# Optimization experiments

Measured on AMD Instinct MI355X. Metric: run time of the kernel, lower is better.

## Reference

```python
import jax, jax.numpy as jnp
import numpy as np

B, T, C, H = 2, 2048, 1024, 16
HD = C // H  # 64


def setup_inputs() -> dict:
    key = jax.random.key(0)
    ks = jax.random.split(key, 5)
    x = jax.random.normal(ks[0], (B, T, C), jnp.float32)
    scale = 0.02
    Wq = jax.random.normal(ks[1], (C, C), jnp.float32) * scale
    Wk = jax.random.normal(ks[2], (C, C), jnp.float32) * scale
    Wv = jax.random.normal(ks[3], (C, C), jnp.float32) * scale
    Wo = jax.random.normal(ks[4], (C, C), jnp.float32) * scale
    # RoPE tables: freqs_cis = exp(i * pos * theta_j), theta_j = 10000^(-2j/HD)
    pos = jnp.arange(T, dtype=jnp.float32)
    theta = 10000.0 ** (-jnp.arange(0, HD, 2, dtype=jnp.float32) / HD)  # [HD/2]
    ang = pos[:, None] * theta[None, :]  # [T, HD/2]
    cos = jnp.cos(ang)
    sin = jnp.sin(ang)
    return {"x": x, "Wq": Wq, "Wk": Wk, "Wv": Wv, "Wo": Wo, "cos": cos, "sin": sin}


def _rope(t, cos, sin):
    # t: [B,T,H,HD]; pairs (even, odd) along last dim form complex numbers
    b, s, h, hd = t.shape
    tr = t.reshape(b, s, h, hd // 2, 2)
    t0, t1 = tr[..., 0], tr[..., 1]
    c = cos[None, :, None, :]  # [1,T,1,HD/2]
    sn = sin[None, :, None, :]
    o0 = t0 * c - t1 * sn
    o1 = t0 * sn + t1 * c
    return jnp.stack([o0, o1], axis=-1).reshape(b, s, h, hd)


def reference(x, Wq, Wk, Wv, Wo, cos, sin):
    b, t, c = x.shape
    h, hd = H, c // H
    q = (x @ Wq.T).reshape(b, t, h, hd)
    k = (x @ Wk.T).reshape(b, t, h, hd)
    v = (x @ Wv.T).reshape(b, t, h, hd)
    q = _rope(q, cos, sin)
    k = _rope(k, cos, sin)
    # explicit causal attention with full TxT score matrix (as in source)
    att = jnp.einsum("bthd,bshd->bhts", q, k) / jnp.sqrt(jnp.float32(hd))
    causal = jnp.tril(jnp.ones((t, t), dtype=bool))
    att = jnp.where(causal[None, None, :, :], att, -jnp.inf)
    att = jax.nn.softmax(att, axis=-1)
    out = jnp.einsum("bhts,bshd->bthd", att, v).reshape(b, t, c)
    return out @ Wo.T
```

## Files before the change

### kernel.cpp

```cpp
#include <hip/hip_runtime.h>
#include <cstdint>
#include <cstddef>


typedef __bf16 bf16;
typedef float  f32x4  __attribute__((ext_vector_type(4)));
typedef __bf16 bf16x4 __attribute__((ext_vector_type(4)));
typedef __bf16 bf16x8 __attribute__((ext_vector_type(8)));

constexpr int Bb = 2, Tt = 2048, Cc = 1024, Hh = 16;
constexpr int Mrows = Bb * Tt;
constexpr int NT = Tt / 64;
constexpr int BM = 128, BN = 128, BK = 64;
constexpr int LDS_ = 72;

#define GLOAD_LDS16(gp, lp)                                                      \
    __builtin_amdgcn_global_load_lds(                                            \
        (const __attribute__((address_space(1))) void*)(gp),                     \
        (__attribute__((address_space(3))) void*)(lp), 16, 0, 0)

#define QUAD_T(v0, v1, v2, v3, c2)                                               \
    {                                                                            \
        float e0 = (c2 & 1) ? v0 : v1, e1 = (c2 & 1) ? v2 : v3;                  \
        e0 = __shfl_xor(e0, 1); e1 = __shfl_xor(e1, 1);                          \
        if (c2 & 1) { v0 = e0; v2 = e1; } else { v1 = e0; v3 = e1; }             \
        float f0 = (c2 & 2) ? v0 : v2, f1 = (c2 & 2) ? v1 : v3;                  \
        f0 = __shfl_xor(f0, 2); f1 = __shfl_xor(f1, 2);                          \
        if (c2 & 2) { v0 = f0; v1 = f1; } else { v2 = f0; v3 = f1; }             \
    }

__global__ __launch_bounds__(256) void convert_k(const float* __restrict__ x,
                                                 const float* __restrict__ Wq,
                                                 const float* __restrict__ Wk,
                                                 const float* __restrict__ Wv,
                                                 const float* __restrict__ Wo,
                                                 const float* __restrict__ cosb,
                                                 const float* __restrict__ sinb,
                                                 bf16* __restrict__ xb,
                                                 bf16* __restrict__ Wqkv,
                                                 bf16* __restrict__ Wob,
                                                 float2* __restrict__ cs)
{
    constexpr size_t M1 = 1024 * 1024;
    if (blockIdx.x >= 4096) {
        int pi = ((blockIdx.x - 4096) * 256 + threadIdx.x) * 8;
#pragma unroll
        for (int u = 0; u < 8; ++u)
            cs[pi + u] = float2{cosb[pi + u], sinb[pi + u]};
        return;
    }
    size_t e = ((size_t)blockIdx.x * 256 + threadIdx.x) * 8;
    const float* src; bf16* dst; float sc = 1.0f;
    if (e < 4 * M1)      { src = x  + e;          dst = xb   + e; }
    else if (e < 5 * M1) { src = Wq + (e - 4*M1); dst = Wqkv + (e - 4*M1);
                           sc = 0.125f * 1.44269504088896f; }
    else if (e < 6 * M1) { src = Wk + (e - 5*M1); dst = Wqkv + M1 + (e - 5*M1); }
    else if (e < 7 * M1) { src = Wv + (e - 6*M1); dst = Wqkv + 2*M1 + (e - 6*M1); }
    else                 { src = Wo + (e - 7*M1); dst = Wob  + (e - 7*M1); }
    float4 v0 = *(const float4*)(src);
    float4 v1 = *(const float4*)(src + 4);
    bf16x8 t;
    t[0] = (bf16)(v0.x*sc); t[1] = (bf16)(v0.y*sc); t[2] = (bf16)(v0.z*sc); t[3] = (bf16)(v0.w*sc);
    t[4] = (bf16)(v1.x*sc); t[5] = (bf16)(v1.y*sc); t[6] = (bf16)(v1.z*sc); t[7] = (bf16)(v1.w*sc);
    *(bf16x8*)dst = t;
}

__global__ __launch_bounds__(256) void gemm_qkv(const bf16* __restrict__ A,
                                                const bf16* __restrict__ W,
                                                bf16* __restrict__ QK,
                                                bf16* __restrict__ Vt,
                                                const float2* __restrict__ cs)
{
    __shared__ bf16 As[BM * BK];
    __shared__ bf16 Ws[BN * BK];
    const int tid  = threadIdx.x;
    const int lane = tid & 63, wave = tid >> 6;
    const int wr = (wave >> 1) * 64, wc = (wave & 1) * 64;
    const int l16 = lane & 15, lq = lane >> 4;
    const int row0 = blockIdx.x * BM, col0 = blockIdx.y * BN;
    const int srow = lane >> 3, scol = (lane & 7) * 8;

    f32x4 acc[4][4];
#pragma unroll
    for (int i = 0; i < 4; ++i)
#pragma unroll
        for (int j = 0; j < 4; ++j) acc[i][j] = f32x4{0.f, 0.f, 0.f, 0.f};

    const bf16* Abase = A + (size_t)(row0 + wave * 8 + srow) * Cc + scol;
    const bf16* Wbase = W + (size_t)(col0 + wave * 8 + srow) * Cc + scol;

    for (int k0 = 0; k0 < Cc; k0 += BK) {
#pragma unroll
        for (int rnd = 0; rnd < 4; ++rnd) {
            const int rr = rnd * 32 + wave * 8;
            GLOAD_LDS16(Abase + (size_t)rnd * 32 * Cc + k0, &As[rr * BK]);
            GLOAD_LDS16(Wbase + (size_t)rnd * 32 * Cc + k0, &Ws[rr * BK]);
        }
        __syncthreads();
#pragma unroll
        for (int ks = 0; ks < BK / 32; ++ks) {
            bf16x8 af[4], bfr[4];
#pragma unroll
            for (int i = 0; i < 4; ++i)
                af[i] = *(const bf16x8*)(&As[(wr + i * 16 + l16) * BK + ks * 32 + lq * 8]);
#pragma unroll
            for (int j = 0; j < 4; ++j)
                bfr[j] = *(const bf16x8*)(&Ws[(wc + j * 16 + l16) * BK + ks * 32 + lq * 8]);
#pragma unroll
            for (int i = 0; i < 4; ++i)
#pragma unroll
                for (int j = 0; j < 4; ++j)
                    acc[i][j] = __builtin_amdgcn_mfma_f32_16x16x32_bf16(
                        af[i], bfr[j], acc[i][j], 0, 0, 0);
        }
        __syncthreads();
    }

    const int c2 = l16 & 3, g4 = (l16 >> 2) * 4;
    if (blockIdx.y < 16) {
#pragma unroll
        for (int i = 0; i < 4; ++i)
#pragma unroll
            for (int j = 0; j < 4; ++j) {
                float v0 = acc[i][j][0], v1 = acc[i][j][1];
                float v2 = acc[i][j][2], v3 = acc[i][j][3];
                QUAD_T(v0, v1, v2, v3, c2);
                const int row = row0 + wr + i * 16 + lq * 4 + c2;
                const int t   = row & (Tt - 1);
                const int colb = wc + j * 16 + g4;
                const int p0   = (colb & 63) >> 1;
                float4 cp = *(const float4*)(&cs[t * 32 + p0]);
                bf16x4 pk;
                pk[0] = (bf16)(v0 * cp.x - v1 * cp.y);
                pk[1] = (bf16)(v0 * cp.y + v1 * cp.x);
                pk[2] = (bf16)(v2 * cp.z - v3 * cp.w);
                pk[3] = (bf16)(v2 * cp.w + v3 * cp.z);
                *(bf16x4*)(&QK[(size_t)row * 2048 + col0 + colb]) = pk;
            }
    } else {
#pragma unroll
        for (int i = 0; i < 4; ++i)
#pragma unroll
            for (int j = 0; j < 4; ++j) {
                const int dfull = col0 - 2048 + wc + j * 16 + l16;
                const int h = dfull >> 6, d = dfull & 63;
                const int row = row0 + wr + i * 16 + lq * 4;
                const int b = row >> 11, t = row & (Tt - 1);
                bf16x4 pk;
                pk[0] = (bf16)acc[i][j][0]; pk[1] = (bf16)acc[i][j][1];
                pk[2] = (bf16)acc[i][j][2]; pk[3] = (bf16)acc[i][j][3];
                *(bf16x4*)(&Vt[((size_t)(b * 16 + h) * 64 + d) * (size_t)Tt + t]) = pk;
            }
    }
}

__global__ __launch_bounds__(256) void gemm_o(const bf16* __restrict__ A,
                                              const bf16* __restrict__ W,
                                              float* __restrict__ Out)
{
    __shared__ bf16 As[BM * BK];
    __shared__ bf16 Ws[64 * BK];
    const int tid  = threadIdx.x;
    const int lane = tid & 63, wave = tid >> 6;
    const int wr = (wave >> 1) * 64, wc = (wave & 1) * 32;
    const int l16 = lane & 15, lq = lane >> 4;
    const int row0 = blockIdx.x * BM, col0 = blockIdx.y * 64;
    const int srow = lane >> 3, scol = (lane & 7) * 8;

    f32x4 acc[4][2];
#pragma unroll
    for (int i = 0; i < 4; ++i)
#pragma unroll
        for (int j = 0; j < 2; ++j) acc[i][j] = f32x4{0.f, 0.f, 0.f, 0.f};

    const bf16* Abase = A + (size_t)(row0 + wave * 8 + srow) * Cc + scol;
    const bf16* Wbase = W + (size_t)(col0 + wave * 8 + srow) * Cc + scol;

    for (int k0 = 0; k0 < Cc; k0 += BK) {
#pragma unroll
        for (int rnd = 0; rnd < 4; ++rnd)
            GLOAD_LDS16(Abase + (size_t)rnd * 32 * Cc + k0, &As[(rnd * 32 + wave * 8) * BK]);
#pragma unroll
        for (int rnd = 0; rnd < 2; ++rnd)
            GLOAD_LDS16(Wbase + (size_t)rnd * 32 * Cc + k0, &Ws[(rnd * 32 + wave * 8) * BK]);
        __syncthreads();
#pragma unroll
        for (int ks = 0; ks < BK / 32; ++ks) {
            bf16x8 af[4], bfr[2];
#pragma unroll
            for (int i = 0; i < 4; ++i)
                af[i] = *(const bf16x8*)(&As[(wr + i * 16 + l16) * BK + ks * 32 + lq * 8]);
#pragma unroll
            for (int j = 0; j < 2; ++j)
                bfr[j] = *(const bf16x8*)(&Ws[(wc + j * 16 + l16) * BK + ks * 32 + lq * 8]);
#pragma unroll
            for (int i = 0; i < 4; ++i)
#pragma unroll
                for (int j = 0; j < 2; ++j)
                    acc[i][j] = __builtin_amdgcn_mfma_f32_16x16x32_bf16(
                        af[i], bfr[j], acc[i][j], 0, 0, 0);
        }
        __syncthreads();
    }
    const int c2 = l16 & 3, g4 = (l16 >> 2) * 4;
#pragma unroll
    for (int i = 0; i < 4; ++i)
#pragma unroll
        for (int j = 0; j < 2; ++j) {
            float v0 = acc[i][j][0], v1 = acc[i][j][1];
            float v2 = acc[i][j][2], v3 = acc[i][j][3];
            QUAD_T(v0, v1, v2, v3, c2);
            const int row = row0 + wr + i * 16 + lq * 4 + c2;
            const int col = col0 + wc + j * 16 + g4;
            *(float4*)(&Out[(size_t)row * Cc + col]) = float4{v0, v1, v2, v3};
        }
}

__global__ __launch_bounds__(256, 4) void attn_k(const bf16* __restrict__ QK,
                                                 const bf16* __restrict__ Vt,
                                                 bf16* __restrict__ O)
{
    __shared__ bf16 Ks[64 * LDS_];
    __shared__ bf16 Vs[64 * LDS_];
    const int tid = threadIdx.x;
    const int wv = tid >> 6, lane = tid & 63;
    const int l16 = lane & 15, lq = lane >> 4;
    const int bh = blockIdx.y, b = bh >> 4, h = bh & 15;
    const int kr = tid >> 2, c0 = (tid & 3) * 16;
    const int pr = 32 * (kr >> 5) + 16 * ((kr >> 2) & 1) + 4 * ((kr >> 3) & 3) + (kr & 3);

    const bf16* kcol = QK + 1024 + (size_t)(b * Tt + kr) * 2048 + h * 64 + c0;
    const bf16* vcol = Vt + ((size_t)bh * 64 + kr) * Tt + c0;

    for (int phase = 0; phase < 2; ++phase) {
        const int qt = phase ? blockIdx.x : (NT - 1 - blockIdx.x);

        const int qglob = qt * 64 + wv * 16 + l16;
        const bf16* qp = QK + (size_t)(b * Tt + qglob) * 2048 + h * 64;
        bf16x8 qf0 = *(const bf16x8*)(qp + lq * 8);
        bf16x8 qf1 = *(const bf16x8*)(qp + 32 + lq * 8);

        uint4 pk0 = *(const uint4*)(kcol);
        uint4 pk1 = *(const uint4*)(kcol + 8);
        uint4 pv0 = *(const uint4*)(vcol);
        uint4 pv1 = *(const uint4*)(vcol + 8);

        float l = 0.f;
        f32x4 o[4];
#pragma unroll
        for (int dt = 0; dt < 4; ++dt) o[dt] = f32x4{0.f, 0.f, 0.f, 0.f};

        for (int t = 0; t <= qt; ++t) {
            *(uint4*)(&Ks[pr * LDS_ + c0])     = pk0;
            *(uint4*)(&Ks[pr * LDS_ + c0 + 8]) = pk1;
            *(uint4*)(&Vs[kr * LDS_ + c0])     = pv0;
            *(uint4*)(&Vs[kr * LDS_ + c0 + 8]) = pv1;
            __syncthreads();
            if (t < qt) {
                const bf16* kn = kcol + (size_t)(t + 1) * 64 * 2048;
                const bf16* vn = vcol + (t + 1) * 64;
                pk0 = *(const uint4*)(kn);
                pk1 = *(const uint4*)(kn + 8);
                pv0 = *(const uint4*)(vn);
                pv1 = *(const uint4*)(vn + 8);
            }

            f32x4 s[4];
#pragma unroll
            for (int mt = 0; mt < 4; ++mt) s[mt] = f32x4{0.f, 0.f, 0.f, 0.f};
#pragma unroll
            for (int mt = 0; mt < 4; ++mt) {
                bf16x8 a0 = *(const bf16x8*)(&Ks[(mt * 16 + l16) * LDS_ + lq * 8]);
                s[mt] = __builtin_amdgcn_mfma_f32_16x16x32_bf16(a0, qf0, s[mt], 0, 0, 0);
            }
#pragma unroll
            for (int mt = 0; mt < 4; ++mt) {
                bf16x8 a1 = *(const bf16x8*)(&Ks[(mt * 16 + l16) * LDS_ + 32 + lq * 8]);
                s[mt] = __builtin_amdgcn_mfma_f32_16x16x32_bf16(a1, qf1, s[mt], 0, 0, 0);
            }
            if (t == qt) {
                const int qloc = wv * 16 + l16;
#pragma unroll
                for (int mt = 0; mt < 4; ++mt)
#pragma unroll
                    for (int r = 0; r < 4; ++r) {
                        int keyl = (mt >> 1) * 32 + lq * 8 + (mt & 1) * 4 + r;
                        if (keyl > qloc) s[mt][r] = -1e30f;
                    }
            }
            bf16x8 pb0, pb1;
#pragma unroll
            for (int mt = 0; mt < 4; ++mt)
#pragma unroll
                for (int r = 0; r < 4; ++r) {
                    float p = exp2f(s[mt][r]);
                    l += p;
                    s[mt][r] = p;
                }
#pragma unroll
            for (int r = 0; r < 4; ++r) {
                pb0[r]     = (bf16)s[0][r];
                pb0[4 + r] = (bf16)s[1][r];
                pb1[r]     = (bf16)s[2][r];
                pb1[4 + r] = (bf16)s[3][r];
            }
#pragma unroll
            for (int dt = 0; dt < 4; ++dt) {
                bf16x8 v0 = *(const bf16x8*)(&Vs[(dt * 16 + l16) * LDS_ + lq * 8]);
                o[dt] = __builtin_amdgcn_mfma_f32_16x16x32_bf16(v0, pb0, o[dt], 0, 0, 0);
            }
#pragma unroll
            for (int dt = 0; dt < 4; ++dt) {
                bf16x8 v1 = *(const bf16x8*)(&Vs[(dt * 16 + l16) * LDS_ + 32 + lq * 8]);
                o[dt] = __builtin_amdgcn_mfma_f32_16x16x32_bf16(v1, pb1, o[dt], 0, 0, 0);
            }
            __syncthreads();
        }
        l += __shfl_xor(l, 16);
        l += __shfl_xor(l, 32);
        float inv = 1.f / l;
        bf16* op = O + (size_t)(b * Tt + qglob) * Cc + h * 64;
#pragma unroll
        for (int dt = 0; dt < 4; ++dt) {
            bf16x4 pk;
#pragma unroll
            for (int r = 0; r < 4; ++r) pk[r] = (bf16)(o[dt][r] * inv);
            *(bf16x4*)(op + dt * 16 + lq * 4) = pk;
        }
    }
}

extern "C" void kernel_launch(void* const* d_in, const int* in_sizes, int n_in,
                              void* d_out, int out_size, void* d_ws, size_t ws_size,
                              hipStream_t stream)
{
    const float* x    = (const float*)d_in[0];
    const float* Wq   = (const float*)d_in[1];
    const float* Wk   = (const float*)d_in[2];
    const float* Wv   = (const float*)d_in[3];
    const float* Wo   = (const float*)d_in[4];
    const float* cosb = (const float*)d_in[5];
    const float* sinb = (const float*)d_in[6];

    constexpr size_t M1 = 1024 * 1024;
    bf16* base = (bf16*)d_ws;
    bf16*   xb   = base;
    bf16*   QK   = base + 4 * M1;
    bf16*   VtG  = base + 12 * M1;
    bf16*   Wqkv = base + 16 * M1;
    bf16*   Wob  = base + 19 * M1;
    float2* csT  = (float2*)(base + 20 * M1);
    bf16*   Ow   = xb;

    convert_k<<<4096 + 32, 256, 0, stream>>>(x, Wq, Wk, Wv, Wo, cosb, sinb,
                                             xb, Wqkv, Wob, csT);

    gemm_qkv<<<dim3(Mrows / BM, 3072 / BN), 256, 0, stream>>>(
        xb, Wqkv, QK, VtG, csT);

    attn_k<<<dim3(NT / 2, Bb * Hh), 256, 0, stream>>>(QK, VtG, Ow);

    gemm_o<<<dim3(Mrows / BM, Cc / 64), 256, 0, stream>>>(Ow, Wob, (float*)d_out);
}
```

Before: 203.2 us.

## Pre-tile GEMM operands into MFMA fragment order for contiguous LDS loads

The convert kernel now writes x, Wqkv and Wo in a blocked layout where each 128x64 (or 64x64) K-tile is contiguous and arranged in MFMA fragment order. The attention kernel writes its output in the same tiled layout. Both GEMMs can then fill LDS with fully contiguous 512-element segments, and fragment reads walk consecutive 16-byte slots. This is meant to remove strided global rows and LDS bank conflicts from the unpadded row-major tiles, at the cost of scattered reads in the convert step and a more complex attention store pattern.

New measurement: 174.6 us. 1.16x faster.

```diff
diff --git a/kernel.cpp b/kernel.cpp
--- a/kernel.cpp
+++ b/kernel.cpp
@@ -11,7 +11,6 @@
 constexpr int Bb = 2, Tt = 2048, Cc = 1024, Hh = 16;
 constexpr int Mrows = Bb * Tt;
 constexpr int NT = Tt / 64;
-constexpr int BM = 128, BN = 128, BK = 64;
 constexpr int LDS_ = 72;
 
 #define GLOAD_LDS16(gp, lp)                                                      \
@@ -41,7 +40,6 @@
                                                  bf16* __restrict__ Wob,
                                                  float2* __restrict__ cs)
 {
-    constexpr size_t M1 = 1024 * 1024;
     if (blockIdx.x >= 4096) {
         int pi = ((blockIdx.x - 4096) * 256 + threadIdx.x) * 8;
 #pragma unroll
@@ -49,14 +47,35 @@
             cs[pi + u] = float2{cosb[pi + u], sinb[pi + u]};
         return;
     }
-    size_t e = ((size_t)blockIdx.x * 256 + threadIdx.x) * 8;
+    uint32_t id = blockIdx.x * 256 + threadIdx.x;
     const float* src; bf16* dst; float sc = 1.0f;
-    if (e < 4 * M1)      { src = x  + e;          dst = xb   + e; }
-    else if (e < 5 * M1) { src = Wq + (e - 4*M1); dst = Wqkv + (e - 4*M1);
-                           sc = 0.125f * 1.44269504088896f; }
-    else if (e < 6 * M1) { src = Wk + (e - 5*M1); dst = Wqkv + M1 + (e - 5*M1); }
-    else if (e < 7 * M1) { src = Wv + (e - 6*M1); dst = Wqkv + 2*M1 + (e - 6*M1); }
-    else                 { src = Wo + (e - 7*M1); dst = Wob  + (e - 7*M1); }
+    if (id < 524288u) {
+        uint32_t tile = id >> 10, slot = id & 1023;
+        uint32_t row = (tile >> 4) * 128 + (slot >> 9) * 64 +
+                       ((slot >> 6) & 3) * 16 + (slot & 15);
+        uint32_t k = (tile & 15) * 64 + ((slot >> 8) & 1) * 32 + ((slot >> 4) & 3) * 8;
+        src = x + (size_t)row * 1024 + k;
+        dst = xb + (size_t)id * 8;
+    } else if (id < 917504u) {
+        uint32_t t2 = id - 524288u;
+        uint32_t tile = t2 >> 10, slot = t2 & 1023;
+        uint32_t n = (tile >> 4) * 128 + (slot >> 9) * 64 +
+                     ((slot >> 6) & 3) * 16 + (slot & 15);
+        uint32_t k = (tile & 15) * 64 + ((slot >> 8) & 1) * 32 + ((slot >> 4) & 3) * 8;
+        if (n < 1024)      { src = Wq + (size_t)n * 1024 + k;
+                             sc = 0.125f * 1.44269504088896f; }
+        else if (n < 2048)   src = Wk + (size_t)(n - 1024) * 1024 + k;
+        else                 src = Wv + (size_t)(n - 2048) * 1024 + k;
+        dst = Wqkv + (size_t)t2 * 8;
+    } else {
+        uint32_t t3 = id - 917504u;
+        uint32_t tile = t3 >> 9, slot = t3 & 511;
+        uint32_t n = (tile >> 4) * 64 + (slot >> 8) * 32 +
+                     ((slot >> 6) & 1) * 16 + (slot & 15);
+        uint32_t k = (tile & 15) * 64 + ((slot >> 7) & 1) * 32 + ((slot >> 4) & 3) * 8;
+        src = Wo + (size_t)n * 1024 + k;
+        dst = Wob + (size_t)t3 * 8;
+    }
     float4 v0 = *(const float4*)(src);
     float4 v1 = *(const float4*)(src + 4);
     bf16x8 t;
@@ -71,14 +90,14 @@
                                                 bf16* __restrict__ Vt,
                                                 const float2* __restrict__ cs)
 {
-    __shared__ bf16 As[BM * BK];
-    __shared__ bf16 Ws[BN * BK];
+    __shared__ bf16 As[8192];
+    __shared__ bf16 Ws[8192];
     const int tid  = threadIdx.x;
     const int lane = tid & 63, wave = tid >> 6;
-    const int wr = (wave >> 1) * 64, wc = (wave & 1) * 64;
+    const int rhw = wave >> 1, chw = wave & 1;
+    const int wr = rhw * 64, wc = chw * 64;
     const int l16 = lane & 15, lq = lane >> 4;
-    const int row0 = blockIdx.x * BM, col0 = blockIdx.y * BN;
-    const int srow = lane >> 3, scol = (lane & 7) * 8;
+    const int row0 = blockIdx.x * 128, col0 = blockIdx.y * 128;
 
     f32x4 acc[4][4];
 #pragma unroll
@@ -86,26 +105,28 @@
 #pragma unroll
         for (int j = 0; j < 4; ++j) acc[i][j] = f32x4{0.f, 0.f, 0.f, 0.f};
 
-    const bf16* Abase = A + (size_t)(row0 + wave * 8 + srow) * Cc + scol;
-    const bf16* Wbase = W + (size_t)(col0 + wave * 8 + srow) * Cc + scol;
-
-    for (int k0 = 0; k0 < Cc; k0 += BK) {
+    const bf16* At = A + (size_t)blockIdx.x * 16 * 8192;
+    const bf16* Wt = W + (size_t)blockIdx.y * 16 * 8192;
+
+    for (int kb = 0; kb < 16; ++kb) {
+        const bf16* at = At + kb * 8192;
+        const bf16* wt = Wt + kb * 8192;
 #pragma unroll
         for (int rnd = 0; rnd < 4; ++rnd) {
-            const int rr = rnd * 32 + wave * 8;
-            GLOAD_LDS16(Abase + (size_t)rnd * 32 * Cc + k0, &As[rr * BK]);
-            GLOAD_LDS16(Wbase + (size_t)rnd * 32 * Cc + k0, &Ws[rr * BK]);
+            const int seg = rnd * 4 + wave;
+            GLOAD_LDS16(at + seg * 512 + lane * 8, &As[seg * 512]);
+            GLOAD_LDS16(wt + seg * 512 + lane * 8, &Ws[seg * 512]);
         }
         __syncthreads();
 #pragma unroll
-        for (int ks = 0; ks < BK / 32; ++ks) {
+        for (int ks = 0; ks < 2; ++ks) {
             bf16x8 af[4], bfr[4];
 #pragma unroll
             for (int i = 0; i < 4; ++i)
-                af[i] = *(const bf16x8*)(&As[(wr + i * 16 + l16) * BK + ks * 32 + lq * 8]);
+                af[i] = *(const bf16x8*)(&As[(rhw * 512 + ks * 256 + i * 64 + lq * 16 + l16) * 8]);
 #pragma unroll
             for (int j = 0; j < 4; ++j)
-                bfr[j] = *(const bf16x8*)(&Ws[(wc + j * 16 + l16) * BK + ks * 32 + lq * 8]);
+                bfr[j] = *(const bf16x8*)(&Ws[(chw * 512 + ks * 256 + j * 64 + lq * 16 + l16) * 8]);
 #pragma unroll
             for (int i = 0; i < 4; ++i)
 #pragma unroll
@@ -158,14 +179,14 @@
                                               const bf16* __restrict__ W,
                                               float* __restrict__ Out)
 {
-    __shared__ bf16 As[BM * BK];
-    __shared__ bf16 Ws[64 * BK];
+    __shared__ bf16 As[8192];
+    __shared__ bf16 Ws[4096];
     const int tid  = threadIdx.x;
     const int lane = tid & 63, wave = tid >> 6;
-    const int wr = (wave >> 1) * 64, wc = (wave & 1) * 32;
+    const int rhw = wave >> 1, chw = wave & 1;
+    const int wr = rhw * 64, wc = chw * 32;
     const int l16 = lane & 15, lq = lane >> 4;
-    const int row0 = blockIdx.x * BM, col0 = blockIdx.y * 64;
-    const int srow = lane >> 3, scol = (lane & 7) * 8;
+    const int row0 = blockIdx.x * 128, col0 = blockIdx.y * 64;
 
     f32x4 acc[4][2];
 #pragma unroll
@@ -173,26 +194,32 @@
 #pragma unroll
         for (int j = 0; j < 2; ++j) acc[i][j] = f32x4{0.f, 0.f, 0.f, 0.f};
 
-    const bf16* Abase = A + (size_t)(row0 + wave * 8 + srow) * Cc + scol;
-    const bf16* Wbase = W + (size_t)(col0 + wave * 8 + srow) * Cc + scol;
-
-    for (int k0 = 0; k0 < Cc; k0 += BK) {
-#pragma unroll
-        for (int rnd = 0; rnd < 4; ++rnd)
-            GLOAD_LDS16(Abase + (size_t)rnd * 32 * Cc + k0, &As[(rnd * 32 + wave * 8) * BK]);
-#pragma unroll
-        for (int rnd = 0; rnd < 2; ++rnd)
-            GLOAD_LDS16(Wbase + (size_t)rnd * 32 * Cc + k0, &Ws[(rnd * 32 + wave * 8) * BK]);
+    const bf16* At = A + (size_t)blockIdx.x * 16 * 8192;
+    const bf16* Wt = W + (size_t)blockIdx.y * 16 * 4096;
+
+    for (int kb = 0; kb < 16; ++kb) {
+        const bf16* at = At + kb * 8192;
+        const bf16* wt = Wt + kb * 4096;
+#pragma unroll
+        for (int rnd = 0; rnd < 4; ++rnd) {
+            const int seg = rnd * 4 + wave;
+            GLOAD_LDS16(at + seg * 512 + lane * 8, &As[seg * 512]);
+        }
+#pragma unroll
+        for (int rnd = 0; rnd < 2; ++rnd) {
+            const int seg = rnd * 4 + wave;
+            GLOAD_LDS16(wt + seg * 512 + lane * 8, &Ws[seg * 512]);
+        }
         __syncthreads();
 #pragma unroll
-        for (int ks = 0; ks < BK / 32; ++ks) {
+        for (int ks = 0; ks < 2; ++ks) {
             bf16x8 af[4], bfr[2];
 #pragma unroll
             for (int i = 0; i < 4; ++i)
-                af[i] = *(const bf16x8*)(&As[(wr + i * 16 + l16) * BK + ks * 32 + lq * 8]);
+                af[i] = *(const bf16x8*)(&As[(rhw * 512 + ks * 256 + i * 64 + lq * 16 + l16) * 8]);
 #pragma unroll
             for (int j = 0; j < 2; ++j)
-                bfr[j] = *(const bf16x8*)(&Ws[(wc + j * 16 + l16) * BK + ks * 32 + lq * 8]);
+                bfr[j] = *(const bf16x8*)(&Ws[(chw * 256 + ks * 128 + j * 64 + lq * 16 + l16) * 8]);
 #pragma unroll
             for (int i = 0; i < 4; ++i)
 #pragma unroll
@@ -319,13 +346,16 @@
         l += __shfl_xor(l, 16);
         l += __shfl_xor(l, 32);
         float inv = 1.f / l;
-        bf16* op = O + (size_t)(b * Tt + qglob) * Cc + h * 64;
+        bf16* obase = O + ((size_t)(b * 16 + (qt >> 1)) * 16 + h) * 8192;
+        const int rh = qt & 1;
 #pragma unroll
         for (int dt = 0; dt < 4; ++dt) {
             bf16x4 pk;
 #pragma unroll
             for (int r = 0; r < 4; ++r) pk[r] = (bf16)(o[dt][r] * inv);
-            *(bf16x4*)(op + dt * 16 + lq * 4) = pk;
+            const int slot = rh * 512 + (dt >> 1) * 256 + wv * 64 +
+                             ((dt & 1) * 2 + (lq >> 1)) * 16 + l16;
+            *(bf16x4*)(obase + slot * 8 + (lq & 1) * 4) = pk;
         }
     }
 }
@@ -355,10 +385,10 @@
     convert_k<<<4096 + 32, 256, 0, stream>>>(x, Wq, Wk, Wv, Wo, cosb, sinb,
                                              xb, Wqkv, Wob, csT);
 
-    gemm_qkv<<<dim3(Mrows / BM, 3072 / BN), 256, 0, stream>>>(
+    gemm_qkv<<<dim3(Mrows / 128, 3072 / 128), 256, 0, stream>>>(
         xb, Wqkv, QK, VtG, csT);
 
     attn_k<<<dim3(NT / 2, Bb * Hh), 256, 0, stream>>>(QK, VtG, Ow);
 
-    gemm_o<<<dim3(Mrows / BM, Cc / 64), 256, 0, stream>>>(Ow, Wob, (float*)d_out);
-}
+    gemm_o<<<dim3(Mrows / 128, Cc / 64), 256, 0, stream>>>(Ow, Wob, (float*)d_out);
+}
```
